# Kernel tuning notes

Hardware: AMD Instinct MI355X
Metric: run time of the kernel (lower is better)

## Reference

```python
import jax, jax.numpy as jnp
import numpy as np

HEADS = 4
DIM_HEAD = 32
SCALE = DIM_HEAD ** -0.5


def setup_inputs() -> dict:
    key = jax.random.key(0)
    ks = jax.random.split(key, 7)
    b, c, h, w = 2, 256, 64, 64
    time_dim = 512
    hidden = HEADS * DIM_HEAD  # 128
    return {
        "x": jax.random.normal(ks[0], (b, c, h, w), jnp.float32),
        "time_emb": jax.random.normal(ks[1], (b, time_dim), jnp.float32),
        "w_mlp": jax.random.normal(ks[2], (2 * c, time_dim), jnp.float32) * 0.02,
        "b_mlp": jax.random.normal(ks[3], (2 * c,), jnp.float32) * 0.02,
        "w_qkv": jax.random.normal(ks[4], (3 * hidden, c), jnp.float32) * 0.05,
        "w_out": jax.random.normal(ks[5], (c, hidden), jnp.float32) * 0.05,
        "b_out": jax.random.normal(ks[6], (c,), jnp.float32) * 0.02,
    }


def reference(x, time_emb, w_mlp, b_mlp, w_qkv, w_out, b_out):
    b, c, h, w = x.shape
    n = h * w
    # FiLM conditioning: SiLU -> Linear -> chunk into (scale, shift)
    t = jax.nn.silu(time_emb) @ w_mlp.T + b_mlp            # [b, 2c]
    scale, shift = jnp.split(t, 2, axis=1)                  # [b, c] each
    x = x * (scale + 1.0)[:, :, None, None] + shift[:, :, None, None]
    # 1x1 conv QKV projection (no bias)
    qkv = jnp.einsum('oc,bchw->bohw', w_qkv, x)             # [b, 3*hidden, h, w]
    q, k, v = jnp.split(qkv, 3, axis=1)                     # [b, hidden, h, w]
    def to_heads(t):
        return t.reshape(b, HEADS, DIM_HEAD, n)             # b h d (x y)
    q, k, v = to_heads(q) * SCALE, to_heads(k), to_heads(v)
    sim = jnp.einsum('bhdi,bhdj->bhij', q, k)               # [b, h, n, n]
    attn = jax.nn.softmax(sim, axis=-1)
    out = jnp.einsum('bhij,bhdj->bhid', attn, v)            # [b, h, n, d]
    # b h (x y) d -> b (h d) x y
    out = out.transpose(0, 1, 3, 2).reshape(b, HEADS * DIM_HEAD, h, w)
    return jnp.einsum('oc,bchw->bohw', w_out, out) + b_out[None, :, None, None]
```

## Files before the change

### kernel.cpp

```cpp
#include <hip/hip_runtime.h>


typedef __bf16 bf16x8 __attribute__((ext_vector_type(8)));
typedef float  f32x16 __attribute__((ext_vector_type(16)));
typedef unsigned uint2v __attribute__((ext_vector_type(2)));

#define MFMA(a, b, c) __builtin_amdgcn_mfma_f32_32x32x16_bf16((a), (b), (c), 0, 0, 0)
#define PLSWAP(a, b) __builtin_amdgcn_permlane32_swap((a), (b), false, false)

static constexpr float kLOG2E = 1.4426950408889634f;
static constexpr float kSCALE = 0.17677669529663687f;

__device__ __forceinline__ unsigned short bf16r(float x) {
  union { float f; unsigned u; } v; v.f = x;
  return (unsigned short)((v.u + 0x7FFFu + ((v.u >> 16) & 1u)) >> 16);
}
__device__ __forceinline__ float fast_silu(float x) {
  return x / (1.0f + __builtin_amdgcn_exp2f(-x * kLOG2E));
}
__device__ __forceinline__ f32x16 zero16() {
  f32x16 z;
#pragma unroll
  for (int i = 0; i < 16; ++i) z[i] = 0.0f;
  return z;
}
__device__ __forceinline__ bf16x8 ld_frag(const unsigned short* p) {
  return *reinterpret_cast<const bf16x8*>(p);
}

__global__ __launch_bounds__(256) void prep(const float* __restrict__ x,
                                            unsigned short* __restrict__ xT,
                                            const float* __restrict__ te,
                                            const float* __restrict__ w_mlp,
                                            const float* __restrict__ b_mlp,
                                            float* __restrict__ fparams) {
  __shared__ unsigned short lds[64][66];
  int bid = blockIdx.x;
  if (bid < 32) {
    int g = bid * 256 + threadIdx.x;
    int pair = g >> 3, ks = g & 7;
    int b = pair >> 9, o = pair & 511;
    const float4* w4 = (const float4*)(w_mlp + (size_t)o * 512 + ks * 64);
    const float4* t4 = (const float4*)(te + (size_t)b * 512 + ks * 64);
    float s = 0.0f;
#pragma unroll 4
    for (int k = 0; k < 16; ++k) {
      float4 wv = w4[k];
      float4 tv = t4[k];
      s += wv.x * fast_silu(tv.x) + wv.y * fast_silu(tv.y) +
           wv.z * fast_silu(tv.z) + wv.w * fast_silu(tv.w);
    }
    s += __shfl_xor(s, 1, 64);
    s += __shfl_xor(s, 2, 64);
    s += __shfl_xor(s, 4, 64);
    if (ks == 0) {
      float t_val = s + b_mlp[o];
      fparams[b * 512 + o] = (o < 256) ? (t_val + 1.0f) : t_val;
    }
    return;
  }
  int bid2 = bid - 32;
  int p0 = (bid2 & 63) * 64;
  int c0 = ((bid2 >> 6) & 3) * 64;
  int b  = bid2 >> 8;
  int t = threadIdx.x;
  int pl = t & 63, cw = t >> 6;
  const float* xb = x + ((size_t)b * 256 + c0) * 4096 + p0;
#pragma unroll
  for (int r = 0; r < 16; ++r) {
    int cl = cw + r * 4;
    lds[pl][cl] = bf16r(xb[(size_t)cl * 4096 + pl]);
  }
  __syncthreads();
  unsigned short* out = xT + ((size_t)b * 4096 + p0) * 256 + c0;
#pragma unroll
  for (int rep = 0; rep < 2; ++rep) {
    int ch = t + rep * 256;
    int pr = ch >> 3, cc = (ch & 7) * 8;
    union { unsigned short u[8]; uint4 v; } pk;
#pragma unroll
    for (int i = 0; i < 8; ++i) pk.u[i] = lds[pr][cc + i];
    *(uint4*)(out + (size_t)pr * 256 + cc) = pk.v;
  }
}

__global__ __launch_bounds__(256) void film2(const float* __restrict__ w_qkv,
                                             const float* __restrict__ fparams,
                                             const float* __restrict__ w_out,
                                             unsigned short* __restrict__ Aeff,
                                             float* __restrict__ qb,
                                             unsigned short* __restrict__ WoBf) {
  int tid = blockIdx.x * 256 + threadIdx.x;
  if (tid < 24576) {
    int row = tid >> 5, cs = tid & 31;
    int b = row / 384, o = row % 384;
    float qs = (o < 128) ? (kSCALE * kLOG2E) : 1.0f;
    const float4* wr  = (const float4*)(w_qkv + (size_t)o * 256);
    const float4* sc4 = (const float4*)(fparams + b * 512);
    const float4* sh4 = (const float4*)(fparams + b * 512 + 256);
    unsigned short* arow = Aeff + ((size_t)b * 384 + o) * 256;
    float acc = 0.0f;
#pragma unroll
    for (int j = 0; j < 2; ++j) {
      int c4 = cs * 2 + j;
      float4 wv = wr[c4], scv = sc4[c4], shv = sh4[c4];
      acc += wv.x * shv.x + wv.y * shv.y + wv.z * shv.z + wv.w * shv.w;
      union { unsigned short u[4]; unsigned long long q; } pk;
      pk.u[0] = bf16r(wv.x * scv.x * qs);
      pk.u[1] = bf16r(wv.y * scv.y * qs);
      pk.u[2] = bf16r(wv.z * scv.z * qs);
      pk.u[3] = bf16r(wv.w * scv.w * qs);
      *(unsigned long long*)(arow + c4 * 4) = pk.q;
    }
    acc += __shfl_xor(acc, 1, 64);
    acc += __shfl_xor(acc, 2, 64);
    acc += __shfl_xor(acc, 4, 64);
    acc += __shfl_xor(acc, 8, 64);
    acc += __shfl_xor(acc, 16, 64);
    if (cs == 0) qb[b * 384 + o] = acc * qs;
  } else {
    int t = tid - 24576;
    const float4* src = (const float4*)(w_out + (size_t)t * 64);
    unsigned short* dst = WoBf + (size_t)t * 64;
#pragma unroll 4
    for (int i = 0; i < 16; ++i) {
      float4 v = src[i];
      union { unsigned short u[4]; unsigned long long q; } pk;
      pk.u[0] = bf16r(v.x); pk.u[1] = bf16r(v.y);
      pk.u[2] = bf16r(v.z); pk.u[3] = bf16r(v.w);
      *(unsigned long long*)(dst + i * 4) = pk.q;
    }
  }
}

__global__ __launch_bounds__(64) void qkv_gemm(const unsigned short* __restrict__ Aeff,
                                               const float* __restrict__ qb,
                                               const unsigned short* __restrict__ xT,
                                               unsigned short* __restrict__ Qb,
                                               unsigned short* __restrict__ Kb,
                                               unsigned short* __restrict__ Vt) {
  int bid = blockIdx.x;
  int o_blk = bid % 12;
  int rest = bid / 12;
  int b = rest & 1, p_blk = rest >> 1;
  int l = threadIdx.x, col = l & 31, hi = l >> 5;

  const unsigned short* Ab = Aeff + ((size_t)b * 384 + o_blk * 32) * 256;
  const unsigned short* Bb = xT + ((size_t)b * 4096 + p_blk * 64) * 256;

  f32x16 acc0 = zero16(), acc1 = zero16();
#pragma unroll
  for (int kc = 0; kc < 256; kc += 16) {
    bf16x8 a0 = ld_frag(Ab + (size_t)col * 256 + kc + hi * 8);
    bf16x8 b0 = ld_frag(Bb + (size_t)col * 256 + kc + hi * 8);
    bf16x8 b1 = ld_frag(Bb + (size_t)(col + 32) * 256 + kc + hi * 8);
    acc0 = MFMA(a0, b0, acc0);
    acc1 = MFMA(a0, b1, acc1);
  }

  int obase = o_blk * 32;
  int sec = obase >> 7;
  int head = (obase & 127) >> 5;
  size_t bh = (size_t)b * 4 + head;
  f32x16 accs[2] = {acc0, acc1};
#pragma unroll
  for (int pt = 0; pt < 2; ++pt) {
    int p = p_blk * 64 + pt * 32 + col;
    f32x16 acc = accs[pt];
    if (sec < 2) {
      unsigned short* dst = (sec == 0 ? Qb : Kb) + (bh * 4096 + p) * 32;
#pragma unroll
      for (int g = 0; g < 4; ++g) {
        int dbase = 8 * g + 4 * hi;
        union { unsigned short u[4]; unsigned long long q; } pk;
#pragma unroll
        for (int r = 0; r < 4; ++r)
          pk.u[r] = bf16r(acc[4 * g + r] + qb[b * 384 + obase + dbase + r]);
        *(unsigned long long*)(dst + dbase) = pk.q;
      }
    } else {
      unsigned short* dst = Vt + bh * 32 * 4096;
#pragma unroll
      for (int reg = 0; reg < 16; ++reg) {
        int d = (reg & 3) + 8 * (reg >> 2) + 4 * hi;
        dst[(size_t)d * 4096 + p] = bf16r(acc[reg] + qb[b * 384 + obase + d]);
      }
    }
  }
}

__device__ __forceinline__ void softmax_pv(f32x16 S, bf16x8 va0, bf16x8 va1,
                                           f32x16& O, float& lsum) {
#pragma unroll
  for (int i = 0; i < 16; ++i) S[i] = __builtin_amdgcn_exp2f(S[i]);
  float s0 = (S[0] + S[1]) + (S[2] + S[3]);
  float s1 = (S[4] + S[5]) + (S[6] + S[7]);
  float s2 = (S[8] + S[9]) + (S[10] + S[11]);
  float s3 = (S[12] + S[13]) + (S[14] + S[15]);
  lsum += (s0 + s1) + (s2 + s3);
  union { __bf16 h[16]; unsigned u[8]; } pu;
#pragma unroll
  for (int i = 0; i < 16; ++i) pu.h[i] = (__bf16)S[i];
  uint2v r0 = PLSWAP(pu.u[0], pu.u[2]);
  uint2v r1 = PLSWAP(pu.u[1], pu.u[3]);
  uint2v r2 = PLSWAP(pu.u[4], pu.u[6]);
  uint2v r3 = PLSWAP(pu.u[5], pu.u[7]);
  union { unsigned u[4]; bf16x8 v; } B0, B1;
  B0.u[0] = r0[0]; B0.u[1] = r1[0]; B0.u[2] = r0[1]; B0.u[3] = r1[1];
  B1.u[0] = r2[0]; B1.u[1] = r3[0]; B1.u[2] = r2[1]; B1.u[3] = r3[1];
  O = MFMA(va0, B0.v, O);
  O = MFMA(va1, B1.v, O);
}

__global__ __launch_bounds__(256, 3) void attn(const unsigned short* __restrict__ Qb,
                                               const unsigned short* __restrict__ Kb,
                                               const unsigned short* __restrict__ Vt,
                                               unsigned short* __restrict__ Ob) {
  __shared__ float Olds[4][2][16][64];
  __shared__ float llds[4][2][64];

  int bid = blockIdx.x;
  int bh = bid >> 6;
  int q0 = (bid & 63) * 64;
  int w = threadIdx.x >> 6;
  int l = threadIdx.x & 63, col = l & 31, hi = l >> 5;

  const unsigned short* Qp = Qb + ((size_t)bh * 4096 + q0) * 32;
  bf16x8 qf0 = ld_frag(Qp + col * 32 + hi * 8);
  bf16x8 qf1 = ld_frag(Qp + col * 32 + 16 + hi * 8);
  bf16x8 qg0 = ld_frag(Qp + (col + 32) * 32 + hi * 8);
  bf16x8 qg1 = ld_frag(Qp + (col + 32) * 32 + 16 + hi * 8);

  const unsigned short* kp =
      Kb + (size_t)bh * 131072 + (size_t)(w * 1024 + col) * 32 + hi * 8;
  const unsigned short* vp =
      Vt + (size_t)bh * 131072 + (size_t)col * 4096 + w * 1024 + hi * 8;

  const f32x16 zc = zero16();
  f32x16 Oa = zero16(), Obb = zero16();
  float lsuma = 0.0f, lsumb = 0.0f;

  for (int it = 0; it < 32; ++it) {
    bf16x8 ka0 = ld_frag(kp);
    bf16x8 ka1 = ld_frag(kp + 16);
    bf16x8 va0 = ld_frag(vp);
    bf16x8 va1 = ld_frag(vp + 16);
    kp += 1024; vp += 32;

    f32x16 Sa = MFMA(ka0, qf0, zc);
    Sa = MFMA(ka1, qf1, Sa);
    f32x16 Sb = MFMA(ka0, qg0, zc);
    Sb = MFMA(ka1, qg1, Sb);

    softmax_pv(Sa, va0, va1, Oa, lsuma);
    softmax_pv(Sb, va0, va1, Obb, lsumb);
  }

  uint2v lra = PLSWAP(__float_as_uint(lsuma), __float_as_uint(lsuma));
  uint2v lrb = PLSWAP(__float_as_uint(lsumb), __float_as_uint(lsumb));
  float lta = __uint_as_float(lra[0]) + __uint_as_float(lra[1]);
  float ltb = __uint_as_float(lrb[0]) + __uint_as_float(lrb[1]);

#pragma unroll
  for (int i = 0; i < 16; ++i) {
    Olds[w][0][i][l] = Oa[i];
    Olds[w][1][i][l] = Obb[i];
  }
  llds[w][0][l] = lta;
  llds[w][1][l] = ltb;
  __syncthreads();

#pragma unroll
  for (int h = 0; h < 2; ++h) {
    float L = (llds[0][h][l] + llds[1][h][l]) + (llds[2][h][l] + llds[3][h][l]);
    float inv = 1.0f / L;
    union { unsigned short u[4]; unsigned long long q; } pk4;
#pragma unroll
    for (int r = 0; r < 4; ++r) {
      int reg = 4 * w + r;
      float v = (Olds[0][h][reg][l] + Olds[1][h][reg][l]) +
                (Olds[2][h][reg][l] + Olds[3][h][reg][l]);
      pk4.u[r] = bf16r(v * inv);
    }
    unsigned short* dst =
        Ob + ((size_t)bh * 4096 + q0 + h * 32 + col) * 32 + 8 * w + 4 * hi;
    *(unsigned long long*)dst = pk4.q;
  }
}

__global__ __launch_bounds__(64) void out_gemm(const unsigned short* __restrict__ Wo,
                                               const unsigned short* __restrict__ Ob,
                                               const float* __restrict__ b_out,
                                               float* __restrict__ out) {
  int bid = blockIdx.x;
  int o_blk = bid & 7;
  int rest = bid >> 3;
  int b = rest & 1, p_blk = rest >> 1;
  int l = threadIdx.x, col = l & 31, hi = l >> 5;

  const unsigned short* Ab = Wo + (size_t)(o_blk * 32) * 128;
  f32x16 acc0 = zero16(), acc1 = zero16();
#pragma unroll
  for (int kc = 0; kc < 128; kc += 16) {
    int head = kc >> 5;
    int doff = (kc & 16) + hi * 8;
    const unsigned short* Bb =
        Ob + (((size_t)b * 4 + head) * 4096 + p_blk * 64) * 32 + doff;
    bf16x8 a0 = ld_frag(Ab + (size_t)col * 128 + kc + hi * 8);
    bf16x8 b0 = ld_frag(Bb + (size_t)col * 32);
    bf16x8 b1 = ld_frag(Bb + (size_t)(col + 32) * 32);
    acc0 = MFMA(a0, b0, acc0);
    acc1 = MFMA(a0, b1, acc1);
  }
  f32x16 accs[2] = {acc0, acc1};
#pragma unroll
  for (int pt = 0; pt < 2; ++pt) {
    int p = p_blk * 64 + pt * 32 + col;
    f32x16 acc = accs[pt];
#pragma unroll
    for (int reg = 0; reg < 16; ++reg) {
      int o = o_blk * 32 + (reg & 3) + 8 * (reg >> 2) + 4 * hi;
      out[((size_t)b * 256 + o) * 4096 + p] = acc[reg] + b_out[o];
    }
  }
}

extern "C" void kernel_launch(void* const* d_in, const int* in_sizes, int n_in,
                              void* d_out, int out_size, void* d_ws, size_t ws_size,
                              hipStream_t stream) {
  const float* x     = (const float*)d_in[0];
  const float* te    = (const float*)d_in[1];
  const float* w_mlp = (const float*)d_in[2];
  const float* b_mlp = (const float*)d_in[3];
  const float* w_qkv = (const float*)d_in[4];
  const float* w_out = (const float*)d_in[5];
  const float* b_out = (const float*)d_in[6];

  char* ws = (char*)d_ws;
  float*          fparams = (float*)(ws + 0);
  float*          qb      = (float*)(ws + 4096);
  unsigned short* Aeff    = (unsigned short*)(ws + 8192);
  unsigned short* WoBf    = (unsigned short*)(ws + 401408);
  unsigned short* xT      = (unsigned short*)(ws + 466944);
  unsigned short* Qb      = (unsigned short*)(ws + 4661248);
  unsigned short* Kb      = (unsigned short*)(ws + 6758400);
  unsigned short* Vt      = (unsigned short*)(ws + 8855552);
  unsigned short* Ob      = (unsigned short*)(ws + 10952704);
  float* out = (float*)d_out;

  hipLaunchKernelGGL(prep, dim3(544), dim3(256), 0, stream, x, xT, te, w_mlp,
                     b_mlp, fparams);
  hipLaunchKernelGGL(film2, dim3(98), dim3(256), 0, stream, w_qkv, fparams, w_out,
                     Aeff, qb, WoBf);
  hipLaunchKernelGGL(qkv_gemm, dim3(1536), dim3(64), 0, stream, Aeff, qb, xT, Qb, Kb, Vt);
  hipLaunchKernelGGL(attn, dim3(512), dim3(256), 0, stream, Qb, Kb, Vt, Ob);
  hipLaunchKernelGGL(out_gemm, dim3(1024), dim3(64), 0, stream, WoBf, Ob, b_out, out);
}
```

Before: 133.2 us.

## Split attention keys across eight waves and halve GEMM tile widths

```diff
diff --git a/kernel.cpp b/kernel.cpp
--- a/kernel.cpp
+++ b/kernel.cpp
@@ -146,45 +146,38 @@
   int l = threadIdx.x, col = l & 31, hi = l >> 5;
 
   const unsigned short* Ab = Aeff + ((size_t)b * 384 + o_blk * 32) * 256;
-  const unsigned short* Bb = xT + ((size_t)b * 4096 + p_blk * 64) * 256;
-
-  f32x16 acc0 = zero16(), acc1 = zero16();
+  const unsigned short* Bb = xT + ((size_t)b * 4096 + p_blk * 32) * 256;
+
+  f32x16 acc = zero16();
 #pragma unroll
   for (int kc = 0; kc < 256; kc += 16) {
     bf16x8 a0 = ld_frag(Ab + (size_t)col * 256 + kc + hi * 8);
     bf16x8 b0 = ld_frag(Bb + (size_t)col * 256 + kc + hi * 8);
-    bf16x8 b1 = ld_frag(Bb + (size_t)(col + 32) * 256 + kc + hi * 8);
-    acc0 = MFMA(a0, b0, acc0);
-    acc1 = MFMA(a0, b1, acc1);
+    acc = MFMA(a0, b0, acc);
   }
 
   int obase = o_blk * 32;
   int sec = obase >> 7;
   int head = (obase & 127) >> 5;
   size_t bh = (size_t)b * 4 + head;
-  f32x16 accs[2] = {acc0, acc1};
-#pragma unroll
-  for (int pt = 0; pt < 2; ++pt) {
-    int p = p_blk * 64 + pt * 32 + col;
-    f32x16 acc = accs[pt];
-    if (sec < 2) {
-      unsigned short* dst = (sec == 0 ? Qb : Kb) + (bh * 4096 + p) * 32;
-#pragma unroll
-      for (int g = 0; g < 4; ++g) {
-        int dbase = 8 * g + 4 * hi;
-        union { unsigned short u[4]; unsigned long long q; } pk;
-#pragma unroll
-        for (int r = 0; r < 4; ++r)
-          pk.u[r] = bf16r(acc[4 * g + r] + qb[b * 384 + obase + dbase + r]);
-        *(unsigned long long*)(dst + dbase) = pk.q;
-      }
-    } else {
-      unsigned short* dst = Vt + bh * 32 * 4096;
-#pragma unroll
-      for (int reg = 0; reg < 16; ++reg) {
-        int d = (reg & 3) + 8 * (reg >> 2) + 4 * hi;
-        dst[(size_t)d * 4096 + p] = bf16r(acc[reg] + qb[b * 384 + obase + d]);
-      }
+  int p = p_blk * 32 + col;
+  if (sec < 2) {
+    unsigned short* dst = (sec == 0 ? Qb : Kb) + (bh * 4096 + p) * 32;
+#pragma unroll
+    for (int g = 0; g < 4; ++g) {
+      int dbase = 8 * g + 4 * hi;
+      union { unsigned short u[4]; unsigned long long q; } pk;
+#pragma unroll
+      for (int r = 0; r < 4; ++r)
+        pk.u[r] = bf16r(acc[4 * g + r] + qb[b * 384 + obase + dbase + r]);
+      *(unsigned long long*)(dst + dbase) = pk.q;
+    }
+  } else {
+    unsigned short* dst = Vt + bh * 32 * 4096;
+#pragma unroll
+    for (int reg = 0; reg < 16; ++reg) {
+      int d = (reg & 3) + 8 * (reg >> 2) + 4 * hi;
+      dst[(size_t)d * 4096 + p] = bf16r(acc[reg] + qb[b * 384 + obase + d]);
     }
   }
 }
@@ -212,12 +205,12 @@
   O = MFMA(va1, B1.v, O);
 }
 
-__global__ __launch_bounds__(256, 3) void attn(const unsigned short* __restrict__ Qb,
+__global__ __launch_bounds__(512, 4) void attn(const unsigned short* __restrict__ Qb,
                                                const unsigned short* __restrict__ Kb,
                                                const unsigned short* __restrict__ Vt,
                                                unsigned short* __restrict__ Ob) {
-  __shared__ float Olds[4][2][16][64];
-  __shared__ float llds[4][2][64];
+  __shared__ float Olds[8][2][16][64];
+  __shared__ float llds[8][2][64];
 
   int bid = blockIdx.x;
   int bh = bid >> 6;
@@ -232,15 +225,15 @@
   bf16x8 qg1 = ld_frag(Qp + (col + 32) * 32 + 16 + hi * 8);
 
   const unsigned short* kp =
-      Kb + (size_t)bh * 131072 + (size_t)(w * 1024 + col) * 32 + hi * 8;
+      Kb + (size_t)bh * 131072 + (size_t)(w * 512 + col) * 32 + hi * 8;
   const unsigned short* vp =
-      Vt + (size_t)bh * 131072 + (size_t)col * 4096 + w * 1024 + hi * 8;
+      Vt + (size_t)bh * 131072 + (size_t)col * 4096 + w * 512 + hi * 8;
 
   const f32x16 zc = zero16();
   f32x16 Oa = zero16(), Obb = zero16();
   float lsuma = 0.0f, lsumb = 0.0f;
 
-  for (int it = 0; it < 32; ++it) {
+  for (int it = 0; it < 16; ++it) {
     bf16x8 ka0 = ld_frag(kp);
     bf16x8 ka1 = ld_frag(kp + 16);
     bf16x8 va0 = ld_frag(vp);
@@ -249,10 +242,10 @@
 
     f32x16 Sa = MFMA(ka0, qf0, zc);
     Sa = MFMA(ka1, qf1, Sa);
+    softmax_pv(Sa, va0, va1, Oa, lsuma);
+
     f32x16 Sb = MFMA(ka0, qg0, zc);
     Sb = MFMA(ka1, qg1, Sb);
-
-    softmax_pv(Sa, va0, va1, Oa, lsuma);
     softmax_pv(Sb, va0, va1, Obb, lsumb);
   }
 
@@ -270,21 +263,25 @@
   llds[w][1][l] = ltb;
   __syncthreads();
 
+  int reg0 = 2 * w;
+  int based = 8 * (w >> 1) + 2 * (w & 1) + 4 * hi;
 #pragma unroll
   for (int h = 0; h < 2; ++h) {
-    float L = (llds[0][h][l] + llds[1][h][l]) + (llds[2][h][l] + llds[3][h][l]);
+    float L = ((llds[0][h][l] + llds[1][h][l]) + (llds[2][h][l] + llds[3][h][l])) +
+              ((llds[4][h][l] + llds[5][h][l]) + (llds[6][h][l] + llds[7][h][l]));
     float inv = 1.0f / L;
-    union { unsigned short u[4]; unsigned long long q; } pk4;
-#pragma unroll
-    for (int r = 0; r < 4; ++r) {
-      int reg = 4 * w + r;
-      float v = (Olds[0][h][reg][l] + Olds[1][h][reg][l]) +
-                (Olds[2][h][reg][l] + Olds[3][h][reg][l]);
-      pk4.u[r] = bf16r(v * inv);
+    float v0 = 0.0f, v1 = 0.0f;
+#pragma unroll
+    for (int i = 0; i < 8; ++i) {
+      v0 += Olds[i][h][reg0][l];
+      v1 += Olds[i][h][reg0 + 1][l];
     }
     unsigned short* dst =
-        Ob + ((size_t)bh * 4096 + q0 + h * 32 + col) * 32 + 8 * w + 4 * hi;
-    *(unsigned long long*)dst = pk4.q;
+        Ob + ((size_t)bh * 4096 + q0 + h * 32 + col) * 32 + based;
+    union { unsigned short u[2]; unsigned q; } pk2;
+    pk2.u[0] = bf16r(v0 * inv);
+    pk2.u[1] = bf16r(v1 * inv);
+    *(unsigned*)dst = pk2.q;
   }
 }
 
@@ -299,29 +296,22 @@
   int l = threadIdx.x, col = l & 31, hi = l >> 5;
 
   const unsigned short* Ab = Wo + (size_t)(o_blk * 32) * 128;
-  f32x16 acc0 = zero16(), acc1 = zero16();
+  f32x16 acc = zero16();
 #pragma unroll
   for (int kc = 0; kc < 128; kc += 16) {
     int head = kc >> 5;
     int doff = (kc & 16) + hi * 8;
     const unsigned short* Bb =
-        Ob + (((size_t)b * 4 + head) * 4096 + p_blk * 64) * 32 + doff;
+        Ob + (((size_t)b * 4 + head) * 4096 + p_blk * 32) * 32 + doff;
     bf16x8 a0 = ld_frag(Ab + (size_t)col * 128 + kc + hi * 8);
     bf16x8 b0 = ld_frag(Bb + (size_t)col * 32);
-    bf16x8 b1 = ld_frag(Bb + (size_t)(col + 32) * 32);
-    acc0 = MFMA(a0, b0, acc0);
-    acc1 = MFMA(a0, b1, acc1);
-  }
-  f32x16 accs[2] = {acc0, acc1};
-#pragma unroll
-  for (int pt = 0; pt < 2; ++pt) {
-    int p = p_blk * 64 + pt * 32 + col;
-    f32x16 acc = accs[pt];
-#pragma unroll
-    for (int reg = 0; reg < 16; ++reg) {
-      int o = o_blk * 32 + (reg & 3) + 8 * (reg >> 2) + 4 * hi;
-      out[((size_t)b * 256 + o) * 4096 + p] = acc[reg] + b_out[o];
-    }
+    acc = MFMA(a0, b0, acc);
+  }
+  int p = p_blk * 32 + col;
+#pragma unroll
+  for (int reg = 0; reg < 16; ++reg) {
+    int o = o_blk * 32 + (reg & 3) + 8 * (reg >> 2) + 4 * hi;
+    out[((size_t)b * 256 + o) * 4096 + p] = acc[reg] + b_out[o];
   }
 }
 
@@ -352,7 +342,7 @@
                      b_mlp, fparams);
   hipLaunchKernelGGL(film2, dim3(98), dim3(256), 0, stream, w_qkv, fparams, w_out,
                      Aeff, qb, WoBf);
-  hipLaunchKernelGGL(qkv_gemm, dim3(1536), dim3(64), 0, stream, Aeff, qb, xT, Qb, Kb, Vt);
-  hipLaunchKernelGGL(attn, dim3(512), dim3(256), 0, stream, Qb, Kb, Vt, Ob);
-  hipLaunchKernelGGL(out_gemm, dim3(1024), dim3(64), 0, stream, WoBf, Ob, b_out, out);
-}
+  hipLaunchKernelGGL(qkv_gemm, dim3(3072), dim3(64), 0, stream, Aeff, qb, xT, Qb, Kb, Vt);
+  hipLaunchKernelGGL(attn, dim3(512), dim3(512), 0, stream, Qb, Kb, Vt, Ob);
+  hipLaunchKernelGGL(out_gemm, dim3(2048), dim3(64), 0, stream, WoBf, Ob, b_out, out);
+}
```

Result: no change. 134.9 us (+1.3%).
